# Optimization experiments

Hardware: AMD Instinct MI355X
Metric: run time of the kernel (lower is better)

The kernel has to match this reference:

```python
import jax, jax.numpy as jnp
import numpy as np

B_IMG = 2
N_PROP = 2000
N_GT = 16
C_FEAT = 256
H_FEAT = 128
W_FEAT = 128
IMG = 1024.0
NUM_CLASSES = 2
BG_THRESH = 0.5          # fg==bg==0.5 -> BETWEEN_THRESHOLDS band is empty
BPI = 512                # batch_size_per_image
NUM_POS_MAX = int(BPI * 0.25)
ENC_W = (1.0, 1.0, 1.0, 1.0, 1.0)
SCALE = 1.0 / 8.0        # feature stride
POOL = 7
SR = 2                   # sampling_ratio
BETA = 1.0 / 9.0
HID = 1024


def _make_boxes(key, shape_prefix, img=IMG):
    kc, ks = jax.random.split(key)
    c = jax.random.uniform(kc, shape_prefix + (2,), minval=0.0, maxval=img)
    s = jax.random.uniform(ks, shape_prefix + (2,), minval=20.0, maxval=200.0)
    lo = jnp.clip(c - 0.5 * s, 0.0, img - 2.0)
    hi = jnp.clip(c + 0.5 * s, lo + 1.0, img)
    return jnp.concatenate([lo, hi], axis=-1)  # [.., x1,y1,x2,y2]


def setup_inputs():
    key = jax.random.key(0)
    ks = jax.random.split(key, 12)
    features = jax.random.normal(ks[0], (B_IMG, C_FEAT, H_FEAT, W_FEAT), dtype=jnp.float32)
    proposals = _make_boxes(ks[1], (B_IMG, N_PROP))
    gt_boxes = _make_boxes(ks[2], (B_IMG, N_GT))
    gt_labels = jax.random.randint(ks[3], (B_IMG, N_GT), 1, NUM_CLASSES, dtype=jnp.int32)
    ka, kb, kt = jax.random.split(ks[4], 3)
    a = jax.random.uniform(ka, (B_IMG, N_GT), minval=10.0, maxval=60.0)
    b = jax.random.uniform(kb, (B_IMG, N_GT), minval=5.0, maxval=30.0)
    th = jax.random.uniform(kt, (B_IMG, N_GT), minval=-np.pi / 2, maxval=np.pi / 2)
    exy = 0.5 * (gt_boxes[..., :2] + gt_boxes[..., 2:])
    gt_ellipses = jnp.stack([a, b, exy[..., 0], exy[..., 1], th], axis=-1)
    d_in = C_FEAT * POOL * POOL
    w1 = jax.random.normal(ks[5], (d_in, HID), dtype=jnp.float32) * 0.02
    b1 = jnp.zeros((HID,), jnp.float32)
    w2 = jax.random.normal(ks[6], (HID, HID), dtype=jnp.float32) * 0.02
    b2 = jnp.zeros((HID,), jnp.float32)
    wc = jax.random.normal(ks[7], (HID, NUM_CLASSES), dtype=jnp.float32) * 0.02
    bc = jnp.zeros((NUM_CLASSES,), jnp.float32)
    wr = jax.random.normal(ks[8], (HID, NUM_CLASSES * 6), dtype=jnp.float32) * 0.02
    br = jnp.zeros((NUM_CLASSES * 6,), jnp.float32)
    return dict(features=features, proposals=proposals, gt_boxes=gt_boxes,
                gt_labels=gt_labels, gt_ellipses=gt_ellipses,
                w1=w1, b1=b1, w2=w2, b2=b2, wc=wc, bc=bc, wr=wr, br=br)


def box_iou(b1, b2):  # [G,4], [P,4] -> [G,P]
    a1 = (b1[:, 2] - b1[:, 0]) * (b1[:, 3] - b1[:, 1])
    a2 = (b2[:, 2] - b2[:, 0]) * (b2[:, 3] - b2[:, 1])
    lt = jnp.maximum(b1[:, None, :2], b2[None, :, :2])
    rb = jnp.minimum(b1[:, None, 2:], b2[None, :, 2:])
    wh = jnp.clip(rb - lt, 0.0)
    inter = wh[..., 0] * wh[..., 1]
    return inter / (a1[:, None] + a2[None, :] - inter)


def encode_ellipses(ell, boxes):  # ell [..,5]=(a,b,cx,cy,theta), boxes [..,4] -> [..,6]
    a, b, ex, ey, th = (ell[..., i] for i in range(5))
    w = jnp.maximum(boxes[..., 2] - boxes[..., 0], 1.0)
    h = jnp.maximum(boxes[..., 3] - boxes[..., 1], 1.0)
    cx = 0.5 * (boxes[..., 0] + boxes[..., 2])
    cy = 0.5 * (boxes[..., 1] + boxes[..., 3])
    wx, wy, wa, wb, wt = ENC_W
    dx = wx * (ex - cx) / w
    dy = wy * (ey - cy) / h
    da = wa * jnp.log(jnp.maximum(2.0 * a, 1e-3) / w)
    db = wb * jnp.log(jnp.maximum(2.0 * b, 1e-3) / h)
    return jnp.stack([dx, dy, da, db, wt * jnp.sin(2.0 * th), wt * jnp.cos(2.0 * th)], axis=-1)


def roi_align(fmap, rois):  # [C,H,W], [R,4] -> [R,C,POOL,POOL]
    C, H, W = fmap.shape
    r = rois * SCALE
    x1, y1, x2, y2 = r[:, 0], r[:, 1], r[:, 2], r[:, 3]
    bw = jnp.maximum(x2 - x1, 1.0) / POOL
    bh = jnp.maximum(y2 - y1, 1.0) / POOL
    S = POOL * SR
    off = (jnp.arange(S, dtype=jnp.float32) + 0.5) / SR  # bin-unit sample offsets
    ys = jnp.clip(y1[:, None] + off[None, :] * bh[:, None], 0.0, H - 1.0)  # [R,S]
    xs = jnp.clip(x1[:, None] + off[None, :] * bw[:, None], 0.0, W - 1.0)
    y0 = jnp.clip(jnp.floor(ys), 0, H - 2).astype(jnp.int32)
    x0 = jnp.clip(jnp.floor(xs), 0, W - 2).astype(jnp.int32)
    ly = ys - y0
    lx = xs - x0
    Ya, Yb = y0[:, :, None], (y0 + 1)[:, :, None]  # [R,S,1]
    Xa, Xb = x0[:, None, :], (x0 + 1)[:, None, :]  # [R,1,S]
    v00 = fmap[:, Ya, Xa]; v01 = fmap[:, Ya, Xb]   # [C,R,S,S]
    v10 = fmap[:, Yb, Xa]; v11 = fmap[:, Yb, Xb]
    wy1 = ly[:, :, None]; wy0 = 1.0 - wy1
    wx1 = lx[:, None, :]; wx0 = 1.0 - wx1
    val = v00 * (wy0 * wx0) + v01 * (wy0 * wx1) + v10 * (wy1 * wx0) + v11 * (wy1 * wx1)
    R = rois.shape[0]
    pooled = val.reshape(C, R, POOL, SR, POOL, SR).mean(axis=(3, 5))
    return pooled.transpose(1, 0, 2, 3)


def reference(features, proposals, gt_boxes, gt_labels, gt_ellipses,
              w1, b1, w2, b2, wc, bc, wr, br):
    B = features.shape[0]
    # add_gt_proposals
    props = jnp.concatenate([proposals, gt_boxes], axis=1)            # [B,P,4]
    # assign_targets_to_proposals: IoU + Matcher (fg=bg=0.5)
    iou = jax.vmap(box_iou)(gt_boxes, props)                          # [B,G,P]
    matched_vals = iou.max(axis=1)
    matches = iou.argmax(axis=1)                                      # [B,P]
    lab = jnp.take_along_axis(gt_labels, matches, axis=1)
    lab = jnp.where(matched_vals < BG_THRESH, 0, lab)                 # background
    # BalancedPositiveNegativeSampler (deterministic, fixed-shape):
    # cap positives at NUM_POS_MAX by random rank, fill rest with random negatives
    rand = jax.random.uniform(jax.random.key(42), lab.shape)
    is_pos = lab > 0
    is_neg = lab == 0
    pos_s = jnp.where(is_pos, rand, -1e9)
    rank = jnp.argsort(jnp.argsort(-pos_s, axis=1), axis=1)
    capped = is_pos & (rank < NUM_POS_MAX)
    prio = jnp.where(capped, rand + 2.0, jnp.where(is_neg, rand, -1e9))
    _, idx = jax.lax.top_k(prio, BPI)                                 # [B,512]
    boxes = jnp.take_along_axis(props, idx[..., None], axis=1)        # [B,512,4]
    labels = jnp.take_along_axis(lab, idx, axis=1)                    # [B,512]
    m = jnp.take_along_axis(matches, idx, axis=1)
    ell = jnp.take_along_axis(gt_ellipses, m[..., None], axis=1)      # [B,512,5]
    targets = encode_ellipses(ell, boxes)                             # [B,512,6]
    # RoIAlign + TwoMLPHead + predictor
    pooled = jax.vmap(roi_align)(features, boxes)                     # [B,512,C,7,7]
    N = B * BPI
    x = pooled.reshape(N, -1)
    x = jax.nn.relu(x @ w1 + b1)
    x = jax.nn.relu(x @ w2 + b2)
    logits = x @ wc + bc                                              # [N,2]
    reg = (x @ wr + br).reshape(N, NUM_CLASSES, 6)
    # ellipse_rcnn_loss
    labels_f = labels.reshape(N)
    t = targets.reshape(N, 6)
    ce = -jnp.take_along_axis(jax.nn.log_softmax(logits, axis=-1), labels_f[:, None], axis=1).mean()
    pred = jnp.take_along_axis(reg, labels_f[:, None, None], axis=1)[:, 0]  # [N,6]
    d = jnp.abs(pred - t)
    sl1 = jnp.where(d < BETA, 0.5 * d * d / BETA, d - 0.5 * BETA)
    reg_loss = jnp.sum(sl1 * (labels_f > 0)[:, None].astype(sl1.dtype)) / N
    return jnp.stack([ce, reg_loss])
```

## Files before the change

kernel.cpp:

```cpp
#include <hip/hip_runtime.h>
#include <hip/hip_bf16.h>
#include <math.h>

#define B_IMG   2
#define N_PROP  2000
#define N_GT    16
#define NPROPS  2016
#define C_FEAT  256
#define H_FEAT  128
#define W_FEAT  128
#define HWF     (H_FEAT*W_FEAT)
#define POOL    7
#define BPI     512
#define NPOSMAX 128
#define NSEL    (B_IMG*BPI)
#define K1      (C_FEAT*POOL*POOL)
#define K1P     12800
#define HID     1024
#define NHEAD   14
#define SPLITK1 16
#define SPLITK2 8

typedef short bf16x8f __attribute__((ext_vector_type(8)));
typedef float f32x4f  __attribute__((ext_vector_type(4)));
typedef short short4v __attribute__((ext_vector_type(4)));

__device__ __forceinline__ void threefry2x32(unsigned k0, unsigned k1,
                                             unsigned& x0, unsigned& x1) {
  unsigned ks[3] = {k0, k1, k0 ^ k1 ^ 0x1BD11BDAu};
  const int R0[4] = {13, 15, 26, 6};
  const int R1[4] = {17, 29, 16, 24};
  x0 += ks[0]; x1 += ks[1];
#pragma unroll
  for (int g = 0; g < 5; g++) {
    const int* rot = (g & 1) ? R1 : R0;
#pragma unroll
    for (int r = 0; r < 4; r++) {
      x0 += x1;
      x1 = (x1 << rot[r]) | (x1 >> (32 - rot[r]));
      x1 ^= x0;
    }
    x0 += ks[(g + 1) % 3];
    x1 += ks[(g + 2) % 3] + (unsigned)(g + 1);
  }
}

#define PRE_SAMPLE   2
#define PRE_TRANS    (PRE_SAMPLE + 2048)
#define PRE_CAST1    (PRE_TRANS + 3136)
#define PRE_CAST0    (PRE_CAST1 + 256)
#define PRE_TOTAL    (PRE_CAST0 + 512)

__global__ __launch_bounds__(256) void k_pre(const float* __restrict__ proposals,
                                             const float* __restrict__ gt_boxes,
                                             const int* __restrict__ gt_labels,
                                             const float* __restrict__ features,
                                             const float* __restrict__ w1,
                                             const float* __restrict__ w2,
                                             float* __restrict__ prio,
                                             int* __restrict__ plab,
                                             int* __restrict__ matches,
                                             __hip_bfloat16* __restrict__ featT,
                                             __hip_bfloat16* __restrict__ W1T,
                                             __hip_bfloat16* __restrict__ W2T,
                                             __hip_bfloat16* __restrict__ Xb) {
  __shared__ __align__(16) char smem[20800];
  int bid = blockIdx.x;
  int tid = threadIdx.x;
  if (bid < PRE_SAMPLE) {
    float* rs    = (float*)smem;
    float* pos_r = (float*)(smem + 8064);
    short* pos_i = (short*)(smem + 16128);
    float* gtb   = (float*)(smem + 20160);
    int*   gtl   = (int*)(smem + 20416);
    int*   cnt   = (int*)(smem + 20480);
    int b = bid;
    int base = b * NPROPS;
    if (tid == 0) *cnt = 0;
    if (tid < N_GT * 4) gtb[tid] = gt_boxes[b * N_GT * 4 + tid];
    if (tid < N_GT) gtl[tid] = gt_labels[b * N_GT + tid];
    __syncthreads();
    for (int i = tid; i < NPROPS; i += 256) {
      unsigned x0 = 0u, x1 = (unsigned)(base + i);
      threefry2x32(0u, 42u, x0, x1);
      unsigned bits = x0 ^ x1;
      float r = __uint_as_float((bits >> 9) | 0x3F800000u) - 1.0f;
      rs[i] = r;
      float p0, p1, p2, p3;
      if (i < N_PROP) {
        const float4 v = *(const float4*)(proposals + ((size_t)b * N_PROP + i) * 4);
        p0 = v.x; p1 = v.y; p2 = v.z; p3 = v.w;
      } else {
        const float* g = &gtb[(i - N_PROP) * 4];
        p0 = g[0]; p1 = g[1]; p2 = g[2]; p3 = g[3];
      }
      float a2 = (p2 - p0) * (p3 - p1);
      float best = -1.0f; int bg = 0;
#pragma unroll
      for (int g = 0; g < N_GT; g++) {
        float g0 = gtb[g*4], g1 = gtb[g*4+1], g2 = gtb[g*4+2], g3 = gtb[g*4+3];
        float a1 = (g2 - g0) * (g3 - g1);
        float wx = fmaxf(fminf(g2, p2) - fmaxf(g0, p0), 0.0f);
        float wy = fmaxf(fminf(g3, p3) - fmaxf(g1, p1), 0.0f);
        float inter = wx * wy;
        float iou = inter / (a1 + a2 - inter);
        if (iou > best) { best = iou; bg = g; }
      }
      matches[base + i] = bg;
      int lab = (best < 0.5f) ? 0 : gtl[bg];
      plab[base + i] = lab;
      if (lab > 0) {
        int s = atomicAdd(cnt, 1);
        pos_i[s] = (short)i; pos_r[s] = r;
      }
    }
    __syncthreads();
    int P = *cnt;
    for (int s = tid; s < P; s += 256) {
      int i = pos_i[s]; float ri = pos_r[s];
      int ch = 0;
      for (int j = 0; j < P; j++) {
        float rj = pos_r[j]; int ij = pos_i[j];
        ch += (rj > ri || (rj == ri && ij < i)) ? 1 : 0;
      }
      rs[i] = (ch < NPOSMAX) ? (ri + 2.0f) : -1000000000.0f;
    }
    __syncthreads();
    for (int i = tid; i < NPROPS; i += 256) prio[base + i] = rs[i];
  } else if (bid < PRE_TRANS) {
    float (*tile)[65] = (float(*)[65])smem;
    int t = bid - PRE_SAMPLE;
    int b = t >> 10;
    int rem = t & 1023;
    int c0 = (rem >> 8) * 64;
    int s0 = (rem & 255) * 64;
    const float* src = features + (size_t)b * C_FEAT * HWF;
    __hip_bfloat16* dst = featT + (size_t)b * HWF * C_FEAT;
    int hw4 = (tid & 15) * 4, cr = tid >> 4;
#pragma unroll
    for (int p = 0; p < 4; p++) {
      int c = cr + p * 16;
      float4 v = *(const float4*)(src + (size_t)(c0 + c) * HWF + s0 + hw4);
      tile[hw4 + 0][c] = v.x; tile[hw4 + 1][c] = v.y;
      tile[hw4 + 2][c] = v.z; tile[hw4 + 3][c] = v.w;
    }
    __syncthreads();
    int c4 = (tid & 15) * 4, hr = tid >> 4;
#pragma unroll
    for (int p = 0; p < 4; p++) {
      int hw = hr + p * 16;
      __hip_bfloat16 o[4] = {__float2bfloat16(tile[hw][c4]), __float2bfloat16(tile[hw][c4+1]),
                             __float2bfloat16(tile[hw][c4+2]), __float2bfloat16(tile[hw][c4+3])};
      *(short4v*)(dst + (size_t)(s0 + hw) * C_FEAT + c0 + c4) = *(short4v*)o;
    }
  } else if (bid < PRE_CAST1) {
    float (*tile)[65] = (float(*)[65])smem;
    int t = bid - PRE_TRANS;
    int p = t >> 6;
    int rem = t & 63;
    int c0 = (rem & 3) * 64;
    int n0 = (rem >> 2) * 64;
    int n4 = (tid & 15) * 4, ig = tid >> 4;
#pragma unroll
    for (int i = ig; i < 64; i += 16) {
      float4 v = *(const float4*)(w1 + (size_t)((c0 + i) * 49 + p) * HID + n0 + n4);
      tile[i][n4] = v.x; tile[i][n4 + 1] = v.y;
      tile[i][n4 + 2] = v.z; tile[i][n4 + 3] = v.w;
    }
    __syncthreads();
    int c4 = (tid & 15) * 4;
#pragma unroll
    for (int i = ig; i < 64; i += 16) {
      __hip_bfloat16 o[4] = {__float2bfloat16(tile[c4][i]), __float2bfloat16(tile[c4 + 1][i]),
                             __float2bfloat16(tile[c4 + 2][i]), __float2bfloat16(tile[c4 + 3][i])};
      *(short4v*)(W1T + (size_t)(n0 + i) * K1P + p * 256 + c0 + c4) = *(short4v*)o;
    }
  } else if (bid < PRE_CAST0) {
    float (*tile)[65] = (float(*)[65])smem;
    int t = bid - PRE_CAST1;
    int c0 = (t & 15) * 64;
    int n0 = (t >> 4) * 64;
    int n4 = (tid & 15) * 4, ig = tid >> 4;
#pragma unroll
    for (int i = ig; i < 64; i += 16) {
      float4 v = *(const float4*)(w2 + (size_t)(c0 + i) * HID + n0 + n4);
      tile[i][n4] = v.x; tile[i][n4 + 1] = v.y;
      tile[i][n4 + 2] = v.z; tile[i][n4 + 3] = v.w;
    }
    __syncthreads();
    int c4 = (tid & 15) * 4;
#pragma unroll
    for (int i = ig; i < 64; i += 16) {
      __hip_bfloat16 o[4] = {__float2bfloat16(tile[c4][i]), __float2bfloat16(tile[c4 + 1][i]),
                             __float2bfloat16(tile[c4 + 2][i]), __float2bfloat16(tile[c4 + 3][i])};
      *(short4v*)(W2T + (size_t)(n0 + i) * HID + c0 + c4) = *(short4v*)o;
    }
  } else {
    int t = bid - PRE_CAST0;
    __hip_bfloat16* buf = (t >> 8) ? W1T : Xb;
    int tt = (t & 255) * 256 + tid;
    int row = tt >> 6;
    int col4 = (tt & 63) << 2;
    short4v z = {0, 0, 0, 0};
    *(short4v*)(buf + (size_t)row * K1P + K1 + col4) = z;
  }
}

__global__ __launch_bounds__(256) void k_select(const float* __restrict__ prio,
    const float* __restrict__ proposals, const float* __restrict__ gt_boxes,
    const int* __restrict__ matches, const int* __restrict__ plab,
    const float* __restrict__ gt_ell,
    float* __restrict__ sel_boxes, int* __restrict__ sel_labels,
    float* __restrict__ targets) {
  int tid = threadIdx.x;
  int wave = tid >> 6, lane = tid & 63;
  int b = blockIdx.y;
  int base = b * NPROPS;
  int i = blockIdx.x * 4 + wave;
  float pi = prio[base + i];
  int rank = 0;
  for (int j = lane; j < NPROPS; j += 64) {
    float pj = prio[base + j];
    rank += (pj > pi || (pj == pi && j < i)) ? 1 : 0;
  }
#pragma unroll
  for (int off = 32; off > 0; off >>= 1) rank += __shfl_down(rank, off);
  if (lane != 0 || rank >= BPI) return;
  int slot = b * BPI + rank;
  float p0, p1, p2, p3;
  if (i < N_PROP) {
    const float* p = proposals + ((size_t)b * N_PROP + i) * 4;
    p0 = p[0]; p1 = p[1]; p2 = p[2]; p3 = p[3];
  } else {
    const float* p = gt_boxes + ((size_t)b * N_GT + (i - N_PROP)) * 4;
    p0 = p[0]; p1 = p[1]; p2 = p[2]; p3 = p[3];
  }
  sel_boxes[slot * 4 + 0] = p0;
  sel_boxes[slot * 4 + 1] = p1;
  sel_boxes[slot * 4 + 2] = p2;
  sel_boxes[slot * 4 + 3] = p3;
  int lb = plab[base + i];
  sel_labels[slot] = lb;
  int m = matches[base + i];
  const float* e = gt_ell + ((size_t)b * N_GT + m) * 5;
  float ea = e[0], eb = e[1], ex = e[2], ey = e[3], eth = e[4];
  float w = fmaxf(p2 - p0, 1.0f), h = fmaxf(p3 - p1, 1.0f);
  float cx = 0.5f * (p0 + p2), cy = 0.5f * (p1 + p3);
  float* t = targets + (size_t)slot * 6;
  t[0] = (ex - cx) / w;
  t[1] = (ey - cy) / h;
  t[2] = logf(fmaxf(2.0f * ea, 0.001f) / w);
  t[3] = logf(fmaxf(2.0f * eb, 0.001f) / h);
  t[4] = sinf(2.0f * eth);
  t[5] = cosf(2.0f * eth);
}

__global__ __launch_bounds__(256) void k_roialign(const __hip_bfloat16* __restrict__ featT,
                                                  const float* __restrict__ sel_boxes,
                                                  __hip_bfloat16* __restrict__ X) {
  int n = blockIdx.x;
  int py = blockIdx.y;
  int t = threadIdx.x;
  int lane = t & 63, sub = t >> 6;
  int c = lane << 2;
  int b = n >> 9;
  const float* bx = sel_boxes + (size_t)n * 4;
  float x1 = bx[0] * 0.125f, y1 = bx[1] * 0.125f;
  float x2 = bx[2] * 0.125f, y2 = bx[3] * 0.125f;
  float bw = fmaxf(x2 - x1, 1.0f) / 7.0f;
  float bh = fmaxf(y2 - y1, 1.0f) / 7.0f;
  const __hip_bfloat16* base = featT + (size_t)b * HWF * C_FEAT;
  int y0A[2]; float lyA[2];
#pragma unroll
  for (int sy = 0; sy < 2; sy++) {
    float off = ((float)(py * 2 + sy) + 0.5f) * 0.5f;
    float ys = fminf(fmaxf(y1 + off * bh, 0.0f), 127.0f);
    int y0 = (int)fminf(fmaxf(floorf(ys), 0.0f), 126.0f);
    y0A[sy] = y0; lyA[sy] = ys - (float)y0;
  }
#pragma unroll
  for (int pass = 0; pass < 2; pass++) {
    int px = sub + (pass << 2);
    if (px >= 7) break;
    float acc[4] = {0.0f, 0.0f, 0.0f, 0.0f};
#pragma unroll
    for (int sx = 0; sx < 2; sx++) {
      float off = ((float)(px * 2 + sx) + 0.5f) * 0.5f;
      float xs = fminf(fmaxf(x1 + off * bw, 0.0f), 127.0f);
      int x0 = (int)fminf(fmaxf(floorf(xs), 0.0f), 126.0f);
      float lx = xs - (float)x0;
#pragma unroll
      for (int sy = 0; sy < 2; sy++) {
        int y0 = y0A[sy]; float ly = lyA[sy];
        const __hip_bfloat16* p = base + ((size_t)(y0 * W_FEAT + x0)) * C_FEAT + c;
        short4v s00 = *(const short4v*)p;
        short4v s01 = *(const short4v*)(p + C_FEAT);
        short4v s10 = *(const short4v*)(p + W_FEAT * C_FEAT);
        short4v s11 = *(const short4v*)(p + W_FEAT * C_FEAT + C_FEAT);
        float w00 = (1.0f - ly) * (1.0f - lx), w01 = (1.0f - ly) * lx;
        float w10 = ly * (1.0f - lx), w11 = ly * lx;
#pragma unroll
        for (int q = 0; q < 4; q++) {
          float v00 = __uint_as_float(((unsigned)(unsigned short)s00[q]) << 16);
          float v01 = __uint_as_float(((unsigned)(unsigned short)s01[q]) << 16);
          float v10 = __uint_as_float(((unsigned)(unsigned short)s10[q]) << 16);
          float v11 = __uint_as_float(((unsigned)(unsigned short)s11[q]) << 16);
          acc[q] += v00 * w00 + v01 * w01 + v10 * w10 + v11 * w11;
        }
      }
    }
    __hip_bfloat16 o[4] = {__float2bfloat16(acc[0] * 0.25f), __float2bfloat16(acc[1] * 0.25f),
                           __float2bfloat16(acc[2] * 0.25f), __float2bfloat16(acc[3] * 0.25f)};
    *(short4v*)&X[(size_t)n * K1P + (size_t)(py * 7 + px) * C_FEAT + c] = *(short4v*)o;
  }
}

__device__ __forceinline__ void gld_lds16(const __hip_bfloat16* g, __hip_bfloat16* l) {
  __builtin_amdgcn_global_load_lds(
      (const __attribute__((address_space(1))) void*)g,
      (__attribute__((address_space(3))) void*)l, 16, 0, 0);
}

template <int MODE>
__global__ __launch_bounds__(MODE == 1 ? 512 : 256)
void k_mfma_gemm(const __hip_bfloat16* __restrict__ A,
                 const __hip_bfloat16* __restrict__ BT,
                 __hip_bfloat16* __restrict__ Pb, int K, int KC) {
  const int AM  = (MODE == 1) ? 256 : 128;
  const int TPB = AM * 2;
  __shared__ __align__(16) __hip_bfloat16 As[AM * 32];
  __shared__ __align__(16) __hip_bfloat16 Bs[128 * 32];
  int lin = blockIdx.x;
  int n0, m0, kz;
  if (MODE == 1) {
    int c = lin & 7, h = lin >> 8, q = (lin >> 3) & 31;
    kz = c + (h << 3);
    n0 = (q & 7) * 128;
    m0 = (q >> 3) * 256;
  } else {
    kz = lin & 7;
    int q = lin >> 3;
    n0 = (q & 7) * 128;
    m0 = (q >> 3) * 128;
  }
  int tid = threadIdx.x;
  int kbeg = kz * KC;
  int srow = tid >> 2;
  int scs  = tid & 3;
  int sg   = scs ^ (srow & 3);
  int scol = sg << 3;
  int wave = tid >> 6, lane = tid & 63;
  const int WMW = AM / 64;
  int wm = (wave % WMW) * 64, wn = (wave / WMW) * 64;
  int lm = lane & 15, quad = lane >> 4;
  int fco = ((quad ^ (lm & 3)) << 3);
  f32x4f acc[4][4] = {};
  for (int k0 = kbeg; k0 < kbeg + KC; k0 += 32) {
    __syncthreads();
#pragma unroll
    for (int r0 = 0; r0 < AM; r0 += TPB / 4)
      gld_lds16(A + (size_t)(m0 + r0 + srow) * K + k0 + scol, &As[(r0 + srow) * 32 + scs * 8]);
#pragma unroll
    for (int r0 = 0; r0 < 128; r0 += TPB / 4)
      gld_lds16(BT + (size_t)(n0 + r0 + srow) * K + k0 + scol, &Bs[(r0 + srow) * 32 + scs * 8]);
    __syncthreads();
    bf16x8f af[4], bf[4];
#pragma unroll
    for (int i = 0; i < 4; i++)
      af[i] = *(const bf16x8f*)&As[(wm + i * 16 + lm) * 32 + fco];
#pragma unroll
    for (int j = 0; j < 4; j++)
      bf[j] = *(const bf16x8f*)&Bs[(wn + j * 16 + lm) * 32 + fco];
#pragma unroll
    for (int i = 0; i < 4; i++)
#pragma unroll
      for (int j = 0; j < 4; j++)
        acc[i][j] = __builtin_amdgcn_mfma_f32_16x16x32_bf16(af[i], bf[j], acc[i][j], 0, 0, 0);
  }
  int tileoff = (MODE == 1) ? (((m0 >> 8) * 8 + (n0 >> 7)) * 32768)
                            : (((m0 >> 7) * 8 + (n0 >> 7)) * 16384);
  __hip_bfloat16* dst = Pb + ((size_t)kz << 20) + tileoff + wave * 4096 + lane * 4;
#pragma unroll
  for (int i = 0; i < 4; i++)
#pragma unroll
    for (int j = 0; j < 4; j++) {
      __hip_bfloat16 o[4] = {__float2bfloat16(acc[i][j][0]), __float2bfloat16(acc[i][j][1]),
                             __float2bfloat16(acc[i][j][2]), __float2bfloat16(acc[i][j][3])};
      *(short4v*)(dst + (i * 4 + j) * 256) = *(short4v*)o;
    }
}

__global__ __launch_bounds__(256) void k_reduce16(const __hip_bfloat16* __restrict__ Pb,
                                                  const float* __restrict__ bias,
                                                  __hip_bfloat16* __restrict__ O) {
  int m4 = blockIdx.x >> 2;
  int n  = (blockIdx.x & 3) * 256 + threadIdx.x;
  int m0i = m4 >> 6, wavem = (m4 >> 4) & 3, i = (m4 >> 2) & 3, quad = m4 & 3;
  int n0i = n >> 7, wn = (n >> 6) & 1, j = (n >> 4) & 3, lm = n & 15;
  int wave = wavem + wn * 4;
  int elem = (m0i * 8 + n0i) * 32768 + wave * 4096 + (i * 4 + j) * 256 + (quad * 16 + lm) * 4;
  float s0 = 0.0f, s1 = 0.0f, s2 = 0.0f, s3 = 0.0f;
#pragma unroll
  for (int z = 0; z < SPLITK1; z++) {
    short4v v = *(const short4v*)(Pb + ((size_t)z << 20) + elem);
    s0 += __uint_as_float(((unsigned)(unsigned short)v[0]) << 16);
    s1 += __uint_as_float(((unsigned)(unsigned short)v[1]) << 16);
    s2 += __uint_as_float(((unsigned)(unsigned short)v[2]) << 16);
    s3 += __uint_as_float(((unsigned)(unsigned short)v[3]) << 16);
  }
  float bv = bias[n];
  int m = m4 * 4;
  O[(size_t)(m + 0) * HID + n] = __float2bfloat16(fmaxf(s0 + bv, 0.0f));
  O[(size_t)(m + 1) * HID + n] = __float2bfloat16(fmaxf(s1 + bv, 0.0f));
  O[(size_t)(m + 2) * HID + n] = __float2bfloat16(fmaxf(s2 + bv, 0.0f));
  O[(size_t)(m + 3) * HID + n] = __float2bfloat16(fmaxf(s3 + bv, 0.0f));
}

__global__ __launch_bounds__(256) void k_reduce_head(const __hip_bfloat16* __restrict__ Pb,
                                                     const float* __restrict__ bias,
                                                     const float* __restrict__ wc,
                                                     const float* __restrict__ bc,
                                                     const float* __restrict__ wr,
                                                     const float* __restrict__ br,
                                                     float* __restrict__ Y) {
  __shared__ float part[4][NHEAD];
  int m = blockIdx.x, tid = threadIdx.x;
  int m0i = m >> 7, wavem = (m >> 6) & 1, fi = (m >> 4) & 3, quad = (m >> 2) & 3, r = m & 3;
  float a[NHEAD];
#pragma unroll
  for (int j = 0; j < NHEAD; j++) a[j] = 0.0f;
#pragma unroll
  for (int nn = 0; nn < 4; nn++) {
    int n = nn * 256 + tid;
    int n0i = n >> 7, wn = (n >> 6) & 1, fj = (n >> 4) & 3, lm = n & 15;
    int wave = wavem + wn * 2;
    int elem = (m0i * 8 + n0i) * 16384 + wave * 4096 + (fi * 4 + fj) * 256
             + (quad * 16 + lm) * 4 + r;
    float s = 0.0f;
#pragma unroll
    for (int z = 0; z < SPLITK2; z++)
      s += __uint_as_float(((unsigned)*(const unsigned short*)(Pb + ((size_t)z << 20) + elem)) << 16);
    float hv = fmaxf(s + bias[n], 0.0f);
    float2 wcv = *(const float2*)(wc + n * 2);
    float4 w0 = *(const float4*)(wr + n * 12);
    float4 w1 = *(const float4*)(wr + n * 12 + 4);
    float4 w2 = *(const float4*)(wr + n * 12 + 8);
    a[0] += hv * wcv.x;  a[1] += hv * wcv.y;
    a[2] += hv * w0.x;   a[3] += hv * w0.y;  a[4] += hv * w0.z;  a[5] += hv * w0.w;
    a[6] += hv * w1.x;   a[7] += hv * w1.y;  a[8] += hv * w1.z;  a[9] += hv * w1.w;
    a[10] += hv * w2.x;  a[11] += hv * w2.y; a[12] += hv * w2.z; a[13] += hv * w2.w;
  }
#pragma unroll
  for (int j = 0; j < NHEAD; j++)
#pragma unroll
    for (int off = 32; off > 0; off >>= 1) a[j] += __shfl_down(a[j], off);
  int wave = tid >> 6, lane = tid & 63;
  if (lane == 0)
#pragma unroll
    for (int j = 0; j < NHEAD; j++) part[wave][j] = a[j];
  __syncthreads();
  if (tid < NHEAD) {
    float v = part[0][tid] + part[1][tid] + part[2][tid] + part[3][tid];
    Y[(size_t)m * NHEAD + tid] = v + ((tid < 2) ? bc[tid] : br[tid - 2]);
  }
}

__global__ __launch_bounds__(1024) void k_loss(const float* __restrict__ Y,
                                               const int* __restrict__ sel_labels,
                                               const float* __restrict__ T,
                                               float* __restrict__ out) {
  __shared__ float sc[1024];
  __shared__ float sr[1024];
  int n = threadIdx.x;
  float l0 = Y[(size_t)n * NHEAD + 0], l1 = Y[(size_t)n * NHEAD + 1];
  int lb = sel_labels[n];
  float mx = fmaxf(l0, l1);
  float lse = mx + logf(expf(l0 - mx) + expf(l1 - mx));
  float ce = lse - (lb ? l1 : l0);
  float reg = 0.0f;
  if (lb > 0) {
    const float beta = 1.0f / 9.0f;
    const float* pr = Y + (size_t)n * NHEAD + 2 + lb * 6;
    const float* t = T + (size_t)n * 6;
#pragma unroll
    for (int j = 0; j < 6; j++) {
      float d = fabsf(pr[j] - t[j]);
      reg += (d < beta) ? (0.5f * d * d / beta) : (d - 0.5f * beta);
    }
  }
  sc[n] = ce; sr[n] = reg;
  __syncthreads();
  for (int s = 512; s > 0; s >>= 1) {
    if (n < s) { sc[n] += sc[n + s]; sr[n] += sr[n + s]; }
    __syncthreads();
  }
  if (n == 0) {
    out[0] = sc[0] * (1.0f / 1024.0f);
    out[1] = sr[0] * (1.0f / 1024.0f);
  }
}

extern "C" void kernel_launch(void* const* d_in, const int* in_sizes, int n_in,
                              void* d_out, int out_size, void* d_ws, size_t ws_size,
                              hipStream_t stream) {
  const float* features  = (const float*)d_in[0];
  const float* proposals = (const float*)d_in[1];
  const float* gt_boxes  = (const float*)d_in[2];
  const int*   gt_labels = (const int*)d_in[3];
  const float* gt_ell    = (const float*)d_in[4];
  const float* w1 = (const float*)d_in[5];
  const float* b1 = (const float*)d_in[6];
  const float* w2 = (const float*)d_in[7];
  const float* b2 = (const float*)d_in[8];
  const float* wc = (const float*)d_in[9];
  const float* bc = (const float*)d_in[10];
  const float* wr = (const float*)d_in[11];
  const float* br = (const float*)d_in[12];
  float* out = (float*)d_out;

  char* ws = (char*)d_ws;
  size_t off = 0;
  auto take = [&](size_t bytes) -> void* {
    void* p = ws + off;
    off = (off + bytes + 255) & ~(size_t)255;
    return p;
  };
  __hip_bfloat16* Pb = (__hip_bfloat16*)take((size_t)SPLITK1 * (1 << 20) * 2);
  __hip_bfloat16* featT = Pb;
  __hip_bfloat16* Xb  = (__hip_bfloat16*)take((size_t)NSEL * K1P * 2);
  float* Y = (float*)Xb;
  __hip_bfloat16* W1T = (__hip_bfloat16*)take((size_t)HID * K1P * 2);
  __hip_bfloat16* W2T = (__hip_bfloat16*)take((size_t)HID * HID * 2);
  __hip_bfloat16* H1b = (__hip_bfloat16*)take((size_t)NSEL * HID * 2);
  int*   matches   = (int*)take((size_t)B_IMG * NPROPS * 4);
  int*   plab      = (int*)take((size_t)B_IMG * NPROPS * 4);
  float* prio      = (float*)take((size_t)B_IMG * NPROPS * 4);
  float* sel_boxes = (float*)take((size_t)NSEL * 4 * 4);
  int*   sel_lab   = (int*)take((size_t)NSEL * 4);
  float* targets   = (float*)take((size_t)NSEL * 6 * 4);

  k_pre<<<PRE_TOTAL, 256, 0, stream>>>(proposals, gt_boxes, gt_labels, features,
                                       w1, w2, prio, plab, matches,
                                       featT, W1T, W2T, Xb);
  k_select<<<dim3(NPROPS / 4, B_IMG), 256, 0, stream>>>(prio, proposals, gt_boxes,
                                                        matches, plab, gt_ell,
                                                        sel_boxes, sel_lab, targets);
  k_roialign<<<dim3(NSEL, POOL), 256, 0, stream>>>(featT, sel_boxes, Xb);

  k_mfma_gemm<1><<<512, 512, 0, stream>>>(Xb, W1T, Pb, K1P, K1P / SPLITK1);
  k_reduce16<<<1024, 256, 0, stream>>>(Pb, b1, H1b);
  k_mfma_gemm<2><<<512, 256, 0, stream>>>(H1b, W2T, Pb, HID, HID / SPLITK2);
  k_reduce_head<<<1024, 256, 0, stream>>>(Pb, b2, wc, bc, wr, br, Y);

  k_loss<<<1, 1024, 0, stream>>>(Y, sel_lab, targets, out);
}
```

Baseline: 246.5 us.

## Replace first FC GEMM with triple-buffered split-K-8 MFMA kernel

Adds a dedicated kernel for the first fully connected layer. It uses 64-wide K tiles, a three-stage LDS ring filled by global-to-LDS loads with explicit vmcnt waits, XOR-swizzled LDS reads and raised wave priority around the MFMA block. Split-K drops from 16 to 8, giving 256 blocks of 512 threads, each handling a longer K range. The goal is to hide load latency and halve the partial sums that must be written and reduced. The cost is fewer blocks and heavy LDS use, which limits each CU to one block.

```diff
diff --git a/kernel.cpp b/kernel.cpp
--- a/kernel.cpp
+++ b/kernel.cpp
@@ -18,7 +18,7 @@
 #define K1P     12800
 #define HID     1024
 #define NHEAD   14
-#define SPLITK1 16
+#define SPLITK1 8
 #define SPLITK2 8
 
 typedef short bf16x8f __attribute__((ext_vector_type(8)));
@@ -321,6 +321,98 @@
       (__attribute__((address_space(3))) void*)l, 16, 0, 0);
 }
 
+#define G1_KC   1600
+#define G1_NKT  25
+#define G1_ABUF 16384
+#define G1_BUFE 24576
+
+__global__ __launch_bounds__(512, 1) void k_gemm1(const __hip_bfloat16* __restrict__ A,
+                                                  const __hip_bfloat16* __restrict__ BT,
+                                                  __hip_bfloat16* __restrict__ Pb) {
+  __shared__ __align__(16) __hip_bfloat16 lds[3 * G1_BUFE];
+  const int lin = blockIdx.x;
+  const int kz = lin >> 5;
+  const int q  = lin & 31;
+  const int m0 = (q >> 3) * 256;
+  const int n0 = (q & 7) * 128;
+  const int kbeg = kz * G1_KC;
+  const int tid = threadIdx.x;
+  const int wave = tid >> 6, lane = tid & 63;
+  const int wm = (wave & 3) * 64, wn = (wave >> 2) * 64;
+  const int lm = lane & 15, quad = lane >> 4;
+
+  f32x4f acc[4][4] = {};
+
+  auto stage = [&](int kt, int sb) {
+    const int kcol = kbeg + kt * 64;
+    __hip_bfloat16* lb = lds + sb * G1_BUFE;
+#pragma unroll
+    for (int u = 0; u < 4; ++u) {
+      int idx = tid + u * 512;
+      int r = idx >> 3, g = (idx & 7) ^ (r & 7);
+      gld_lds16(A + (size_t)(m0 + r) * K1P + kcol + g * 8, lb + idx * 8);
+    }
+#pragma unroll
+    for (int u = 0; u < 2; ++u) {
+      int idx = tid + u * 512;
+      int r = idx >> 3, g = (idx & 7) ^ (r & 7);
+      gld_lds16(BT + (size_t)(n0 + r) * K1P + kcol + g * 8, lb + G1_ABUF + idx * 8);
+    }
+  };
+
+  stage(0, 0);
+  stage(1, 1);
+  asm volatile("s_waitcnt vmcnt(6)" ::: "memory");
+  __builtin_amdgcn_s_barrier();
+
+  int buf = 0;
+  for (int kt = 0; kt < G1_NKT; ++kt) {
+    int sb = buf + 2; if (sb >= 3) sb -= 3;
+    if (kt + 2 < G1_NKT) stage(kt + 2, sb);
+    const __hip_bfloat16* Ab = lds + buf * G1_BUFE;
+    const __hip_bfloat16* Bb = Ab + G1_ABUF;
+    bf16x8f af[4][2], bf[4][2];
+#pragma unroll
+    for (int i = 0; i < 4; ++i)
+#pragma unroll
+      for (int s = 0; s < 2; ++s)
+        af[i][s] = *(const bf16x8f*)(Ab + (wm + i * 16 + lm) * 64 +
+                                     (((s << 2) + quad) ^ (lm & 7)) * 8);
+#pragma unroll
+    for (int j = 0; j < 4; ++j)
+#pragma unroll
+      for (int s = 0; s < 2; ++s)
+        bf[j][s] = *(const bf16x8f*)(Bb + (wn + j * 16 + lm) * 64 +
+                                     (((s << 2) + quad) ^ (lm & 7)) * 8);
+    __builtin_amdgcn_s_setprio(1);
+#pragma unroll
+    for (int s = 0; s < 2; ++s)
+#pragma unroll
+      for (int i = 0; i < 4; ++i)
+#pragma unroll
+        for (int j = 0; j < 4; ++j)
+          acc[i][j] = __builtin_amdgcn_mfma_f32_16x16x32_bf16(af[i][s], bf[j][s], acc[i][j], 0, 0, 0);
+    __builtin_amdgcn_s_setprio(0);
+    if (kt < G1_NKT - 1) {
+      if (kt < G1_NKT - 2) asm volatile("s_waitcnt vmcnt(6)" ::: "memory");
+      else                 asm volatile("s_waitcnt vmcnt(0)" ::: "memory");
+      __builtin_amdgcn_s_barrier();
+    }
+    buf = (buf == 2) ? 0 : buf + 1;
+  }
+
+  int tileoff = ((m0 >> 8) * 8 + (n0 >> 7)) * 32768;
+  __hip_bfloat16* dst = Pb + ((size_t)kz << 20) + tileoff + wave * 4096 + lane * 4;
+#pragma unroll
+  for (int i = 0; i < 4; ++i)
+#pragma unroll
+    for (int j = 0; j < 4; ++j) {
+      __hip_bfloat16 o[4] = {__float2bfloat16(acc[i][j][0]), __float2bfloat16(acc[i][j][1]),
+                             __float2bfloat16(acc[i][j][2]), __float2bfloat16(acc[i][j][3])};
+      *(short4v*)(dst + (i * 4 + j) * 256) = *(short4v*)o;
+    }
+}
+
 template <int MODE>
 __global__ __launch_bounds__(MODE == 1 ? 512 : 256)
 void k_mfma_gemm(const __hip_bfloat16* __restrict__ A,
@@ -333,15 +425,15 @@
   int lin = blockIdx.x;
   int n0, m0, kz;
   if (MODE == 1) {
-    int c = lin & 7, h = lin >> 8, q = (lin >> 3) & 31;
+    int c = lin & 7, h = lin >> 8, qq = (lin >> 3) & 31;
     kz = c + (h << 3);
-    n0 = (q & 7) * 128;
-    m0 = (q >> 3) * 256;
+    n0 = (qq & 7) * 128;
+    m0 = (qq >> 3) * 256;
   } else {
     kz = lin & 7;
-    int q = lin >> 3;
-    n0 = (q & 7) * 128;
-    m0 = (q >> 3) * 128;
+    int qq = lin >> 3;
+    n0 = (qq & 7) * 128;
+    m0 = (qq >> 3) * 128;
   }
   int tid = threadIdx.x;
   int kbeg = kz * KC;
@@ -525,7 +617,7 @@
     off = (off + bytes + 255) & ~(size_t)255;
     return p;
   };
-  __hip_bfloat16* Pb = (__hip_bfloat16*)take((size_t)SPLITK1 * (1 << 20) * 2);
+  __hip_bfloat16* Pb = (__hip_bfloat16*)take((size_t)16 * (1 << 20) * 2);
   __hip_bfloat16* featT = Pb;
   __hip_bfloat16* Xb  = (__hip_bfloat16*)take((size_t)NSEL * K1P * 2);
   float* Y = (float*)Xb;
@@ -547,7 +639,7 @@
                                                         sel_boxes, sel_lab, targets);
   k_roialign<<<dim3(NSEL, POOL), 256, 0, stream>>>(featT, sel_boxes, Xb);
 
-  k_mfma_gemm<1><<<512, 512, 0, stream>>>(Xb, W1T, Pb, K1P, K1P / SPLITK1);
+  k_gemm1<<<256, 512, 0, stream>>>(Xb, W1T, Pb);
   k_reduce16<<<1024, 256, 0, stream>>>(Pb, b1, H1b);
   k_mfma_gemm<2><<<512, 256, 0, stream>>>(H1b, W2T, Pb, HID, HID / SPLITK2);
   k_reduce_head<<<1024, 256, 0, stream>>>(Pb, b2, wc, bc, wr, br, Y);
```

Result: no change. 245.6 us (-0.4%).
